# Performance work log

Measured on AMD Instinct MI355X. Metric: run time of the kernel, lower is better.

Reference implementation:

```python
import jax, jax.numpy as jnp
import numpy as np

GRID = 256
N_PER_ORG = 1536
N = 3 * N_PER_ORG
D = 256
H = 512
RADIUS = 5.0
FI_THRESHOLD = 0.5


def setup_inputs() -> dict:
    key = jax.random.key(0)
    ks = jax.random.split(key, 12)
    states = jax.random.normal(ks[0], (N, D), jnp.float32) * 0.1
    energies = jax.random.uniform(ks[1], (N,), jnp.float32, 0.2, 0.8)
    # radial resource distribution as in _init_resources
    c = GRID // 2
    yy, xx = jnp.meshgrid(jnp.arange(GRID, dtype=jnp.float32), jnp.arange(GRID, dtype=jnp.float32), indexing='ij')
    dist = jnp.sqrt((xx - c) ** 2 + (yy - c) ** 2)
    max_dist = jnp.sqrt(2.0) * GRID / 2
    resource_grid = jnp.maximum(0.0, 1.0 - dist / max_dist)
    sD, sH = 1.0 / np.sqrt(D), 1.0 / np.sqrt(H)
    W_out = jax.random.normal(ks[2], (3, D, H), jnp.float32) * sD
    W_in = jax.random.normal(ks[3], (3, D, H), jnp.float32) * sD
    W1 = jax.random.normal(ks[4], (3, D, H), jnp.float32) * sD
    W2 = jax.random.normal(ks[5], (3, H, D), jnp.float32) * sH
    b_out = jnp.zeros((3, H), jnp.float32)
    b_in = jnp.zeros((3, H), jnp.float32)
    b1 = jnp.zeros((3, H), jnp.float32)
    b2 = jnp.zeros((3, D), jnp.float32)
    roles = jax.random.randint(ks[6], (N,), 0, 3, jnp.int32)
    org_ids = jnp.repeat(jnp.arange(3, dtype=jnp.int32), N_PER_ORG)
    positions = jax.random.randint(ks[7], (N, 2), 0, GRID, jnp.int32)
    return {"states": states, "energies": energies, "resource_grid": resource_grid,
            "W_out": W_out, "b_out": b_out, "W_in": W_in, "b_in": b_in,
            "W1": W1, "b1": b1, "W2": W2, "b2": b2,
            "roles": roles, "org_ids": org_ids, "positions": positions}


def reference(states, energies, resource_grid, W_out, b_out, W_in, b_in, W1, b1, W2, b2, roles, org_ids, positions):
    n = states.shape[0]
    idx = jnp.arange(n)
    pos = positions.astype(jnp.float32)
    # neighbor mask: dist <= RADIUS, excluding self  [N,N]
    d2 = jnp.sum((pos[:, None, :] - pos[None, :, :]) ** 2, axis=-1)
    nb = (d2 <= RADIUS * RADIUS) & (~jnp.eye(n, dtype=bool))
    same_org = nb & (org_ids[:, None] == org_ids[None, :])
    other_org = nb & (org_ids[:, None] != org_ids[None, :])
    role0 = roles == 0
    role1 = roles == 1
    same_mass = jnp.sum(same_org & role0[None, :], axis=-1).astype(jnp.float32)
    same_fi = jnp.sum(same_org & role1[None, :], axis=-1).astype(jnp.float32)
    enemy_fi = jnp.sum(other_org & role1[None, :], axis=-1).astype(jnp.float32)
    # bidirectional influence (per-organism behavior nets)
    A = jnp.tanh(jnp.einsum('nd,kdh->knh', states, W_out) + b_out[:, None, :])  # [3,N,H]
    B = jnp.tanh(jnp.einsum('nd,kdh->knh', states, W_in) + b_in[:, None, :])
    scores = jnp.einsum('knh,kmh->knm', A, B) / np.sqrt(H)  # [3,N,N]
    sel_out = scores[org_ids, idx]                      # out_ij = score_{org_i}[i,j]
    sel_in = scores.transpose(0, 2, 1)[org_ids, idx]    # in_ij  = score_{org_i}[j,i]
    cnt = jnp.sum(same_org, axis=-1).astype(jnp.float32)
    denom = jnp.maximum(cnt, 1.0)
    out_mean = jnp.sum(sel_out * same_org, axis=-1) / denom
    in_mean = jnp.sum(sel_in * same_org, axis=-1) / denom
    has_nb = cnt > 0
    net_influence = jnp.where(has_nb, out_mean - in_mean, 0.0)
    # self similarity MLP, per-organism
    H1 = jnp.tanh(jnp.einsum('nd,kdh->knh', states, W1) + b1[:, None, :])
    SP = jnp.einsum('knh,khd->knd', H1, W2) + b2[:, None, :]
    sp = SP[org_ids, idx]  # [N,D]
    new_states = jnp.where(has_nb[:, None], states + 0.1 * sp, states)
    # energy update
    res = resource_grid[positions[:, 1], positions[:, 0]]
    e_fi = energies + 0.03 * same_mass + 0.02 * res - 0.04 * enemy_fi - 0.01
    e_mass = energies * 0.98 + 0.02 * (same_fi > 0).astype(jnp.float32) + 0.01 * res - 0.02 * enemy_fi
    new_energy = jnp.clip(jnp.where(role1, e_fi, e_mass), 0.0, 1.0)
    # role transitions (deterministic part of step())
    can_fi = (new_energy > FI_THRESHOLD) & (same_mass >= 2) & (same_fi == 0) & (enemy_fi == 0)
    r0_new = jnp.where(can_fi, 1, 0)
    loses = (same_mass < 1) | (new_energy < 0.15) | (enemy_fi > same_fi + 1)
    r1_new = jnp.where(loses, 0, 1)
    new_role_idx = jnp.where(role0, r0_new, jnp.where(role1, r1_new, roles))
    new_roles = jax.nn.one_hot(new_role_idx, 3, dtype=jnp.float32)
    return jnp.concatenate([new_states, net_influence[:, None], new_energy[:, None], new_roles], axis=-1)
```

## Files before the change

### kernel.cpp

```cpp
#include <hip/hip_runtime.h>

#define M_AG   4608
#define NPO    1536
#define D_DIM  256
#define H_DIM  512
#define NBIG   1536
#define GRID_SZ 256
#define NB_CAP 48

typedef __attribute__((ext_vector_type(8))) short short8;
typedef __attribute__((ext_vector_type(4))) float f32x4;
typedef unsigned short ushort_t;
typedef unsigned long long u64;

struct Args {
  const float *S, *W_out, *W_in, *W1, *W2, *b_out, *b_in, *b1, *b2;
  const float *energies, *resource_grid;
  const int *roles, *positions;
  ushort_t *Sc, *Wc, *W2c, *Abf, *Bbf, *Hc;
  int4 *stats;
  int *nbl;
  float *out;
};

__device__ __forceinline__ ushort_t f2bf(float f) {
  unsigned int u = __builtin_bit_cast(unsigned int, f);
  unsigned int r = (u + 0x7FFFu + ((u >> 16) & 1u)) >> 16;
  return (ushort_t)r;
}
__device__ __forceinline__ float bf2f(ushort_t u) {
  return __builtin_bit_cast(float, (unsigned int)u << 16);
}
__device__ __forceinline__ float tanh_fast(float x) {
  float e = __builtin_amdgcn_exp2f(x * 2.8853900817779268f);
  return 1.f - 2.f * __builtin_amdgcn_rcpf(e + 1.f);
}
__device__ __forceinline__ void gl_lds16(const ushort_t* g, ushort_t* l) {
  __builtin_amdgcn_global_load_lds(
      (const __attribute__((address_space(1))) unsigned int*)g,
      (__attribute__((address_space(3))) unsigned int*)l, 16, 0, 0);
}
#define VM0_BAR() do { asm volatile("s_waitcnt vmcnt(0)" ::: "memory"); \
                       __builtin_amdgcn_s_barrier(); } while (0)

__device__ __forceinline__ void pack_task(const Args& A, int task) {
  const int t = threadIdx.x;
  if (task < 576) {
    int idx = task * 256 + t;
    int kc = idx / M_AG, m = idx - kc * M_AG;
    const float* p = A.S + (size_t)m * D_DIM + kc * 8;
    ushort_t* d = A.Sc + (size_t)idx * 8;
#pragma unroll
    for (int j = 0; j < 8; ++j) d[j] = f2bf(p[j]);
  } else if (task < 1152) {
    int idx = (task - 576) * 256 + t;
    int org = idx / (32 * NBIG);
    int rem = idx - org * (32 * NBIG);
    int kc = rem / NBIG, n = rem - kc * NBIG;
    int which = n >> 9, nl = n & 511;
    const float* Wsel = (which == 0 ? A.W_out : which == 1 ? A.W_in : A.W1);
    const float* p = Wsel + (size_t)org * (D_DIM * H_DIM) + (size_t)kc * 8 * H_DIM + nl;
    ushort_t* d = A.Wc + (size_t)idx * 8;
#pragma unroll
    for (int j = 0; j < 8; ++j) d[j] = f2bf(p[(size_t)j * H_DIM]);
  } else {
    int idx = (task - 1152) * 256 + t;
    int org = idx / (64 * D_DIM);
    int rem = idx - org * (64 * D_DIM);
    int kc = rem >> 8, n = rem & 255;
    const float* p = A.W2 + (size_t)org * (H_DIM * D_DIM) + (size_t)kc * 8 * D_DIM + n;
    ushort_t* d = A.W2c + (size_t)idx * 8;
#pragma unroll
    for (int j = 0; j < 8; ++j) d[j] = f2bf(p[(size_t)j * D_DIM]);
  }
}

__device__ __forceinline__ void scan_task(const Args& A, int stask, char* smem) {
  const int t = threadIdx.x;
  int* pk = (int*)smem;
  u64* r0m = (u64*)(smem + 18432);
  u64* r1m = r0m + 72;
  for (int j = t; j < M_AG; j += 256) {
    int2 p2 = ((const int2*)A.positions)[j];
    pk[j] = p2.x | (p2.y << 8) | (A.roles[j] << 16);
  }
  __syncthreads();
  const int w = t >> 6, l = t & 63;
  for (int g = w; g < 72; g += 4) {
    int rj = pk[g * 64 + l] >> 16;
    u64 m0 = __ballot(rj == 0);
    u64 m1 = __ballot(rj == 1);
    if (l == 0) { r0m[g] = m0; r1m[g] = m1; }
  }
  __syncthreads();
  const int base_i = stask * 8;
#pragma unroll
  for (int rep = 0; rep < 2; ++rep) {
    const int i = base_i + rep * 4 + w;
    const int pi = pk[i];
    const int xi = pi & 255, yi = (pi >> 8) & 255;
    const int org = (i >= NPO) + (i >= 2 * NPO);
    const int olo = org * NPO, ohi = olo + NPO;
    int nbn = 0, mass = 0, fi = 0, enemy = 0;
    for (int bs = olo; bs < ohi; bs += 64) {
      int j = bs + l;
      int pj = pk[j];
      int dx = (pj & 255) - xi, dy = ((pj >> 8) & 255) - yi;
      bool in_r = (dx * dx + dy * dy <= 25) && (j != i);
      u64 ms = __ballot(in_r);
      if (ms) {
        int g = bs >> 6;
        mass += __popcll(ms & r0m[g]);
        fi   += __popcll(ms & r1m[g]);
        if (in_r) {
          int slot = nbn + __popcll(ms & ((1ull << l) - 1ull));
          if (slot < NB_CAP) A.nbl[i * NB_CAP + slot] = j;
        }
        nbn += __popcll(ms);
      }
    }
#pragma unroll
    for (int half = 0; half < 2; ++half) {
      const int lo = half ? ohi : 0;
      const int hi = half ? M_AG : olo;
      for (int bs = lo; bs < hi; bs += 64) {
        int pj = pk[bs + l];
        int dx = (pj & 255) - xi, dy = ((pj >> 8) & 255) - yi;
        u64 ms = __ballot(dx * dx + dy * dy <= 25);
        enemy += __popcll(ms & r1m[bs >> 6]);
      }
    }
    if (l == 0) A.stats[i] = make_int4(nbn, mass, fi, enemy);
  }
}

__device__ __forceinline__ void gemm_tile(const Args& A, int tix, char* smem) {
  ushort_t* As = (ushort_t*)smem;
  ushort_t* Bs = (ushort_t*)(smem + 16384);
  const int t = threadIdx.x;
  const int w = t >> 6, l = t & 63;
  const int wm = w >> 1, wn = w & 1;
  const int lr = l & 15, lg = l >> 4;
  const int bx = tix % 24, by = tix / 24;
  const int n0 = bx * 64, m0 = by * 64;
  const int org = m0 / NPO;
  const int which = n0 >> 9, nlb = n0 & 511;
  const int g0 = t >> 6, r0 = t & 63, g1 = 4 + g0;
  const size_t wbase = (size_t)org * 32;

  f32x4 acc[2][2] = {};

  auto STAGE = [&](int s, int p) {
    const int kg = s * 8;
    ushort_t* Ad = As + p * 4096;
    ushort_t* Bd = Bs + p * 4096;
    gl_lds16(A.Sc + ((size_t)(kg + g0) * M_AG + m0 + r0) * 8, Ad + (size_t)t * 8);
    gl_lds16(A.Sc + ((size_t)(kg + g1) * M_AG + m0 + r0) * 8, Ad + (size_t)(t + 256) * 8);
    gl_lds16(A.Wc + ((wbase + kg + g0) * NBIG + n0 + r0) * 8, Bd + (size_t)t * 8);
    gl_lds16(A.Wc + ((wbase + kg + g1) * NBIG + n0 + r0) * 8, Bd + (size_t)(t + 256) * 8);
  };

  STAGE(0, 0);
  VM0_BAR();
  for (int s = 0; s < 4; ++s) {
    const int p = s & 1;
    if (s < 3) STAGE(s + 1, p ^ 1);
    const short8* Ap = (const short8*)(As + p * 4096);
    const short8* Bp = (const short8*)(Bs + p * 4096);
    short8 af[2][2], bf_[2][2];
#pragma unroll
    for (int k2 = 0; k2 < 2; ++k2) {
#pragma unroll
      for (int mi = 0; mi < 2; ++mi)
        af[mi][k2] = Ap[(k2 * 4 + lg) * 64 + wm * 32 + mi * 16 + lr];
#pragma unroll
      for (int ni = 0; ni < 2; ++ni)
        bf_[ni][k2] = Bp[(k2 * 4 + lg) * 64 + wn * 32 + ni * 16 + lr];
    }
#pragma unroll
    for (int mi = 0; mi < 2; ++mi)
#pragma unroll
      for (int ni = 0; ni < 2; ++ni)
#pragma unroll
        for (int k2 = 0; k2 < 2; ++k2)
          acc[mi][ni] = __builtin_amdgcn_mfma_f32_16x16x32_bf16(
              af[mi][k2], bf_[ni][k2], acc[mi][ni], 0, 0, 0);
    VM0_BAR();
  }

  const float* bias = (which == 0 ? A.b_out : which == 1 ? A.b_in : A.b1) + (size_t)org * H_DIM;
  ushort_t* dst = (which == 0) ? A.Abf : A.Bbf;
#pragma unroll
  for (int ni = 0; ni < 2; ++ni) {
    const int nl = nlb + wn * 32 + ni * 16 + lr;
    const float bb = bias[nl];
#pragma unroll
    for (int mi = 0; mi < 2; ++mi)
#pragma unroll
      for (int r = 0; r < 4; ++r) {
        const int row = m0 + wm * 32 + mi * 16 + lg * 4 + r;
        ushort_t hv = f2bf(tanh_fast(acc[mi][ni][r] + bb));
        if (which < 2) dst[(size_t)row * H_DIM + nl] = hv;
        else           A.Hc[((size_t)(nl >> 3) * M_AG + row) * 8 + (nl & 7)] = hv;
      }
  }
}

__device__ __forceinline__ void sp_tile(const Args& A, int s_ix, char* smem) {
  ushort_t* As = (ushort_t*)smem;
  ushort_t* Bs = (ushort_t*)(smem + 16384);
  const int t = threadIdx.x;
  const int w = t >> 6, l = t & 63;
  const int wm = w >> 1, wn = w & 1;
  const int lr = l & 15, lg = l >> 4;
  const int bx = s_ix & 3, by = s_ix >> 2;
  const int n0 = bx * 64, m0 = by * 64;
  const int org = m0 / NPO;
  const int g0 = t >> 6, r0 = t & 63, g1 = 4 + g0;
  const size_t w2base = (size_t)org * 64;

  f32x4 acc[2][2] = {};

  auto STAGE = [&](int s, int p) {
    const int kg = s * 8;
    ushort_t* Ad = As + p * 4096;
    ushort_t* Bd = Bs + p * 4096;
    gl_lds16(A.Hc + ((size_t)(kg + g0) * M_AG + m0 + r0) * 8, Ad + (size_t)t * 8);
    gl_lds16(A.Hc + ((size_t)(kg + g1) * M_AG + m0 + r0) * 8, Ad + (size_t)(t + 256) * 8);
    gl_lds16(A.W2c + ((w2base + kg + g0) * D_DIM + n0 + r0) * 8, Bd + (size_t)t * 8);
    gl_lds16(A.W2c + ((w2base + kg + g1) * D_DIM + n0 + r0) * 8, Bd + (size_t)(t + 256) * 8);
  };

  STAGE(0, 0);
  VM0_BAR();
  for (int s = 0; s < 8; ++s) {
    const int p = s & 1;
    if (s < 7) STAGE(s + 1, p ^ 1);
    const short8* Ap = (const short8*)(As + p * 4096);
    const short8* Bp = (const short8*)(Bs + p * 4096);
    short8 af[2][2], bf_[2][2];
#pragma unroll
    for (int k2 = 0; k2 < 2; ++k2) {
#pragma unroll
      for (int mi = 0; mi < 2; ++mi)
        af[mi][k2] = Ap[(k2 * 4 + lg) * 64 + wm * 32 + mi * 16 + lr];
#pragma unroll
      for (int ni = 0; ni < 2; ++ni)
        bf_[ni][k2] = Bp[(k2 * 4 + lg) * 64 + wn * 32 + ni * 16 + lr];
    }
#pragma unroll
    for (int mi = 0; mi < 2; ++mi)
#pragma unroll
      for (int ni = 0; ni < 2; ++ni)
#pragma unroll
        for (int k2 = 0; k2 < 2; ++k2)
          acc[mi][ni] = __builtin_amdgcn_mfma_f32_16x16x32_bf16(
              af[mi][k2], bf_[ni][k2], acc[mi][ni], 0, 0, 0);
    VM0_BAR();
  }
#pragma unroll
  for (int mi = 0; mi < 2; ++mi)
#pragma unroll
    for (int r = 0; r < 4; ++r) {
      const int row = m0 + wm * 32 + mi * 16 + lg * 4 + r;
      const bool has = A.stats[row].x > 0;
#pragma unroll
      for (int ni = 0; ni < 2; ++ni) {
        const int col = n0 + wn * 32 + ni * 16 + lr;
        const float sv = A.S[(size_t)row * D_DIM + col];
        A.out[(size_t)row * 261 + col] =
            has ? sv + 0.1f * (acc[mi][ni][r] + A.b2[org * D_DIM + col]) : sv;
      }
    }
}

__device__ __forceinline__ void finish4(const Args& A, int ftask) {
  const int t = threadIdx.x;
  const int w = t >> 6, l = t & 63;
  const int i = ftask * 4 + w;
  const int4 stv = A.stats[i];
  const int cnt = stv.x, mass = stv.y, fi = stv.z, enemy = stv.w;
  float po = 0.f, pin = 0.f;
  if (cnt > 0) {
    short8 av = *(const short8*)(A.Abf + (size_t)i * H_DIM + l * 8);
    short8 bv = *(const short8*)(A.Bbf + (size_t)i * H_DIM + l * 8);
    const int nn = cnt < NB_CAP ? cnt : NB_CAP;
    for (int s = 0; s < nn; ++s) {
      const int j = A.nbl[i * NB_CAP + s];
      short8 bj = *(const short8*)(A.Bbf + (size_t)j * H_DIM + l * 8);
      short8 aj = *(const short8*)(A.Abf + (size_t)j * H_DIM + l * 8);
#pragma unroll
      for (int k2 = 0; k2 < 8; ++k2) {
        po  += bf2f((ushort_t)av[k2]) * bf2f((ushort_t)bj[k2]);
        pin += bf2f((ushort_t)bv[k2]) * bf2f((ushort_t)aj[k2]);
      }
    }
#pragma unroll
    for (int m2 = 1; m2 < 64; m2 <<= 1) {
      po  += __shfl_xor(po,  m2, 64);
      pin += __shfl_xor(pin, m2, 64);
    }
  }
  if (l == 0) {
    const float denom = fmaxf((float)cnt, 1.0f);
    const float invs = 0.044194173824159216f;
    const float ni_v = (cnt > 0) ? (po - pin) * invs / denom : 0.f;
    const int2 p2 = ((const int2*)A.positions)[i];
    const float res = A.resource_grid[p2.y * GRID_SZ + p2.x];
    const float e = A.energies[i];
    const int r = A.roles[i];
    float e_fi   = e + 0.03f * (float)mass + 0.02f * res - 0.04f * (float)enemy - 0.01f;
    float e_mass = e * 0.98f + 0.02f * ((fi > 0) ? 1.f : 0.f) + 0.01f * res - 0.02f * (float)enemy;
    float ne = (r == 1) ? e_fi : e_mass;
    ne = fminf(fmaxf(ne, 0.f), 1.f);
    const bool can_fi = (ne > 0.5f) && (mass >= 2) && (fi == 0) && (enemy == 0);
    const bool loses = (mass < 1) || (ne < 0.15f) || (enemy > fi + 1);
    const int nr = (r == 0) ? (can_fi ? 1 : 0) : ((r == 1) ? (loses ? 0 : 1) : r);
    float* orow = A.out + (size_t)i * 261;
    orow[256] = ni_v;
    orow[257] = ne;
    orow[258] = (nr == 0) ? 1.f : 0.f;
    orow[259] = (nr == 1) ? 1.f : 0.f;
    orow[260] = (nr == 2) ? 1.f : 0.f;
  }
}

__global__ __launch_bounds__(256) void k_p1(Args A) {
  pack_task(A, blockIdx.x);
}
__global__ __launch_bounds__(256) void k_p2(Args A) {
  __shared__ __align__(16) char smem[32768];
  if (blockIdx.x < 1728) gemm_tile(A, blockIdx.x, smem);
  else                   scan_task(A, blockIdx.x - 1728, smem);
}
__global__ __launch_bounds__(256) void k_p3(Args A) {
  __shared__ __align__(16) char smem[32768];
  if (blockIdx.x < 288) sp_tile(A, blockIdx.x, smem);
  else                  finish4(A, blockIdx.x - 288);
}

extern "C" void kernel_launch(void* const* d_in, const int* in_sizes, int n_in,
                              void* d_out, int out_size, void* d_ws, size_t ws_size,
                              hipStream_t stream) {
  char* ws = (char*)d_ws;
  Args a;
  a.S             = (const float*)d_in[0];
  a.energies      = (const float*)d_in[1];
  a.resource_grid = (const float*)d_in[2];
  a.W_out         = (const float*)d_in[3];
  a.b_out         = (const float*)d_in[4];
  a.W_in          = (const float*)d_in[5];
  a.b_in          = (const float*)d_in[6];
  a.W1            = (const float*)d_in[7];
  a.b1            = (const float*)d_in[8];
  a.W2            = (const float*)d_in[9];
  a.b2            = (const float*)d_in[10];
  a.roles         = (const int*)d_in[11];
  a.positions     = (const int*)d_in[13];
  a.Sc    = (ushort_t*)(ws);
  a.Wc    = (ushort_t*)(ws +  2359296);
  a.W2c   = (ushort_t*)(ws +  4718592);
  a.Hc    = (ushort_t*)(ws +  5505024);
  a.Abf   = (ushort_t*)(ws + 10223616);
  a.Bbf   = (ushort_t*)(ws + 14942208);
  a.stats = (int4*)    (ws + 19660800);
  a.nbl   = (int*)     (ws + 19734528);
  a.out   = (float*)d_out;

  k_p1<<<1344, 256, 0, stream>>>(a);
  k_p2<<<2304, 256, 0, stream>>>(a);
  k_p3<<<1440, 256, 0, stream>>>(a);
}
```

Baseline: 53.06 us.

## Fuse per-row self-similarity MLP with H1 in LDS and regroup kernels

Replaces the separate W1 GEMM tiles and the SP GEMM with one row-block MLP task. Each block computes tanh(S·W1) in chunks, stages H1 in LDS and immediately multiplies by W2, so the H1 workspace round trip through global memory disappears. The neighbour scan moves into the prep kernel alongside packing, and finalize gets its own kernel. The trade-off is that only 144 fused blocks run, and they read weights straight from global without LDS double buffering, which could leave a long tail.

```diff
diff --git a/kernel.cpp b/kernel.cpp
--- a/kernel.cpp
+++ b/kernel.cpp
@@ -17,7 +17,7 @@
   const float *S, *W_out, *W_in, *W1, *W2, *b_out, *b_in, *b1, *b2;
   const float *energies, *resource_grid;
   const int *roles, *positions;
-  ushort_t *Sc, *Wc, *W2c, *Abf, *Bbf, *Hc;
+  ushort_t *Sc, *Wc, *W2c, *Abf, *Bbf;
   int4 *stats;
   int *nbl;
   float *out;
@@ -141,7 +141,7 @@
   const int w = t >> 6, l = t & 63;
   const int wm = w >> 1, wn = w & 1;
   const int lr = l & 15, lg = l >> 4;
-  const int bx = tix % 24, by = tix / 24;
+  const int bx = tix & 15, by = tix >> 4;
   const int n0 = bx * 64, m0 = by * 64;
   const int org = m0 / NPO;
   const int which = n0 >> 9, nlb = n0 & 511;
@@ -188,7 +188,7 @@
     VM0_BAR();
   }
 
-  const float* bias = (which == 0 ? A.b_out : which == 1 ? A.b_in : A.b1) + (size_t)org * H_DIM;
+  const float* bias = (which == 0 ? A.b_out : A.b_in) + (size_t)org * H_DIM;
   ushort_t* dst = (which == 0) ? A.Abf : A.Bbf;
 #pragma unroll
   for (int ni = 0; ni < 2; ++ni) {
@@ -199,77 +199,115 @@
 #pragma unroll
       for (int r = 0; r < 4; ++r) {
         const int row = m0 + wm * 32 + mi * 16 + lg * 4 + r;
-        ushort_t hv = f2bf(tanh_fast(acc[mi][ni][r] + bb));
-        if (which < 2) dst[(size_t)row * H_DIM + nl] = hv;
-        else           A.Hc[((size_t)(nl >> 3) * M_AG + row) * 8 + (nl & 7)] = hv;
-      }
-  }
-}
-
-__device__ __forceinline__ void sp_tile(const Args& A, int s_ix, char* smem) {
-  ushort_t* As = (ushort_t*)smem;
-  ushort_t* Bs = (ushort_t*)(smem + 16384);
+        dst[(size_t)row * H_DIM + nl] = f2bf(tanh_fast(acc[mi][ni][r] + bb));
+      }
+  }
+}
+
+__device__ __forceinline__ void row_mlp(const Args& A, int blk, char* smem) {
+  ushort_t* Sres = (ushort_t*)smem;
+  ushort_t* H1c  = (ushort_t*)(smem + 16384);
   const int t = threadIdx.x;
   const int w = t >> 6, l = t & 63;
-  const int wm = w >> 1, wn = w & 1;
   const int lr = l & 15, lg = l >> 4;
-  const int bx = s_ix & 3, by = s_ix >> 2;
-  const int n0 = bx * 64, m0 = by * 64;
+  const int wn = w;
+  const int m0 = blk * 32;
   const int org = m0 / NPO;
-  const int g0 = t >> 6, r0 = t & 63, g1 = 4 + g0;
-  const size_t w2base = (size_t)org * 64;
-
-  f32x4 acc[2][2] = {};
-
-  auto STAGE = [&](int s, int p) {
-    const int kg = s * 8;
-    ushort_t* Ad = As + p * 4096;
-    ushort_t* Bd = Bs + p * 4096;
-    gl_lds16(A.Hc + ((size_t)(kg + g0) * M_AG + m0 + r0) * 8, Ad + (size_t)t * 8);
-    gl_lds16(A.Hc + ((size_t)(kg + g1) * M_AG + m0 + r0) * 8, Ad + (size_t)(t + 256) * 8);
-    gl_lds16(A.W2c + ((w2base + kg + g0) * D_DIM + n0 + r0) * 8, Bd + (size_t)t * 8);
-    gl_lds16(A.W2c + ((w2base + kg + g1) * D_DIM + n0 + r0) * 8, Bd + (size_t)(t + 256) * 8);
-  };
-
-  STAGE(0, 0);
+
+#pragma unroll
+  for (int j = 0; j < 4; ++j) {
+    int c = j * 256 + t;
+    int kg = c >> 5, row = c & 31;
+    gl_lds16(A.Sc + ((size_t)kg * M_AG + m0 + row) * 8, Sres + (size_t)c * 8);
+  }
   VM0_BAR();
-  for (int s = 0; s < 8; ++s) {
-    const int p = s & 1;
-    if (s < 7) STAGE(s + 1, p ^ 1);
-    const short8* Ap = (const short8*)(As + p * 4096);
-    const short8* Bp = (const short8*)(Bs + p * 4096);
-    short8 af[2][2], bf_[2][2];
-#pragma unroll
-    for (int k2 = 0; k2 < 2; ++k2) {
+
+  f32x4 sp[2][4] = {};
+  const short8* Sp = (const short8*)Sres;
+  const short8* Hp = (const short8*)H1c;
+
+#pragma unroll
+  for (int c = 0; c < 4; ++c) {
+    const int cbase = c * 128;
+    f32x4 a1[2][2] = {};
+#pragma unroll
+    for (int s = 0; s < 4; ++s) {
+      short8 bq[2][2];
+#pragma unroll
+      for (int ni = 0; ni < 2; ++ni)
+#pragma unroll
+        for (int k2 = 0; k2 < 2; ++k2)
+          bq[ni][k2] = *(const short8*)(A.Wc +
+              ((size_t)(org * 32 + s * 8 + k2 * 4 + lg) * NBIG +
+               1024 + cbase + wn * 32 + ni * 16 + lr) * 8);
+      short8 af[2][2];
 #pragma unroll
       for (int mi = 0; mi < 2; ++mi)
-        af[mi][k2] = Ap[(k2 * 4 + lg) * 64 + wm * 32 + mi * 16 + lr];
-#pragma unroll
-      for (int ni = 0; ni < 2; ++ni)
-        bf_[ni][k2] = Bp[(k2 * 4 + lg) * 64 + wn * 32 + ni * 16 + lr];
-    }
+#pragma unroll
+        for (int k2 = 0; k2 < 2; ++k2)
+          af[mi][k2] = Sp[(s * 8 + k2 * 4 + lg) * 32 + mi * 16 + lr];
+#pragma unroll
+      for (int mi = 0; mi < 2; ++mi)
+#pragma unroll
+        for (int ni = 0; ni < 2; ++ni)
+#pragma unroll
+          for (int k2 = 0; k2 < 2; ++k2)
+            a1[mi][ni] = __builtin_amdgcn_mfma_f32_16x16x32_bf16(
+                af[mi][k2], bq[ni][k2], a1[mi][ni], 0, 0, 0);
+    }
+    __syncthreads();
 #pragma unroll
     for (int mi = 0; mi < 2; ++mi)
 #pragma unroll
-      for (int ni = 0; ni < 2; ++ni)
+      for (int ni = 0; ni < 2; ++ni) {
+        const int col = wn * 32 + ni * 16 + lr;
+        const float bb = A.b1[org * H_DIM + cbase + col];
+#pragma unroll
+        for (int r = 0; r < 4; ++r) {
+          const int row = mi * 16 + lg * 4 + r;
+          H1c[((size_t)(col >> 3) * 32 + row) * 8 + (col & 7)] =
+              f2bf(tanh_fast(a1[mi][ni][r] + bb));
+        }
+      }
+    __syncthreads();
+#pragma unroll
+    for (int s2 = 0; s2 < 2; ++s2) {
+      short8 bq[4][2];
+#pragma unroll
+      for (int ni = 0; ni < 4; ++ni)
 #pragma unroll
         for (int k2 = 0; k2 < 2; ++k2)
-          acc[mi][ni] = __builtin_amdgcn_mfma_f32_16x16x32_bf16(
-              af[mi][k2], bf_[ni][k2], acc[mi][ni], 0, 0, 0);
-    VM0_BAR();
+          bq[ni][k2] = *(const short8*)(A.W2c +
+              ((size_t)(org * 64 + c * 16 + s2 * 8 + k2 * 4 + lg) * D_DIM +
+               wn * 64 + ni * 16 + lr) * 8);
+      short8 af[2][2];
+#pragma unroll
+      for (int mi = 0; mi < 2; ++mi)
+#pragma unroll
+        for (int k2 = 0; k2 < 2; ++k2)
+          af[mi][k2] = Hp[(s2 * 8 + k2 * 4 + lg) * 32 + mi * 16 + lr];
+#pragma unroll
+      for (int mi = 0; mi < 2; ++mi)
+#pragma unroll
+        for (int ni = 0; ni < 4; ++ni)
+#pragma unroll
+          for (int k2 = 0; k2 < 2; ++k2)
+            sp[mi][ni] = __builtin_amdgcn_mfma_f32_16x16x32_bf16(
+                af[mi][k2], bq[ni][k2], sp[mi][ni], 0, 0, 0);
+    }
   }
 #pragma unroll
   for (int mi = 0; mi < 2; ++mi)
 #pragma unroll
     for (int r = 0; r < 4; ++r) {
-      const int row = m0 + wm * 32 + mi * 16 + lg * 4 + r;
+      const int row = m0 + mi * 16 + lg * 4 + r;
       const bool has = A.stats[row].x > 0;
 #pragma unroll
-      for (int ni = 0; ni < 2; ++ni) {
-        const int col = n0 + wn * 32 + ni * 16 + lr;
+      for (int ni = 0; ni < 4; ++ni) {
+        const int col = wn * 64 + ni * 16 + lr;
         const float sv = A.S[(size_t)row * D_DIM + col];
         A.out[(size_t)row * 261 + col] =
-            has ? sv + 0.1f * (acc[mi][ni][r] + A.b2[org * D_DIM + col]) : sv;
+            has ? sv + 0.1f * (sp[mi][ni][r] + A.b2[org * D_DIM + col]) : sv;
       }
     }
 }
@@ -325,18 +363,18 @@
   }
 }
 
-__global__ __launch_bounds__(256) void k_p1(Args A) {
-  pack_task(A, blockIdx.x);
-}
-__global__ __launch_bounds__(256) void k_p2(Args A) {
+__global__ __launch_bounds__(256) void k_prep(Args A) {
+  __shared__ __align__(16) char smem[19584];
+  if (blockIdx.x < 1344) pack_task(A, blockIdx.x);
+  else                   scan_task(A, blockIdx.x - 1344, smem);
+}
+__global__ __launch_bounds__(256) void k_main(Args A) {
   __shared__ __align__(16) char smem[32768];
-  if (blockIdx.x < 1728) gemm_tile(A, blockIdx.x, smem);
-  else                   scan_task(A, blockIdx.x - 1728, smem);
-}
-__global__ __launch_bounds__(256) void k_p3(Args A) {
-  __shared__ __align__(16) char smem[32768];
-  if (blockIdx.x < 288) sp_tile(A, blockIdx.x, smem);
-  else                  finish4(A, blockIdx.x - 288);
+  if (blockIdx.x < 144) row_mlp(A, blockIdx.x, smem);
+  else                  gemm_tile(A, blockIdx.x - 144, smem);
+}
+__global__ __launch_bounds__(256) void k_fin(Args A) {
+  finish4(A, blockIdx.x);
 }
 
 extern "C" void kernel_launch(void* const* d_in, const int* in_sizes, int n_in,
@@ -360,14 +398,13 @@
   a.Sc    = (ushort_t*)(ws);
   a.Wc    = (ushort_t*)(ws +  2359296);
   a.W2c   = (ushort_t*)(ws +  4718592);
-  a.Hc    = (ushort_t*)(ws +  5505024);
-  a.Abf   = (ushort_t*)(ws + 10223616);
-  a.Bbf   = (ushort_t*)(ws + 14942208);
-  a.stats = (int4*)    (ws + 19660800);
-  a.nbl   = (int*)     (ws + 19734528);
+  a.Abf   = (ushort_t*)(ws +  5505024);
+  a.Bbf   = (ushort_t*)(ws + 10223616);
+  a.stats = (int4*)    (ws + 14942208);
+  a.nbl   = (int*)     (ws + 15015936);
   a.out   = (float*)d_out;
 
-  k_p1<<<1344, 256, 0, stream>>>(a);
-  k_p2<<<2304, 256, 0, stream>>>(a);
-  k_p3<<<1440, 256, 0, stream>>>(a);
-}
+  k_prep<<<1920, 256, 0, stream>>>(a);
+  k_main<<<1296, 256, 0, stream>>>(a);
+  k_fin <<<1152, 256, 0, stream>>>(a);
+}
```

Result: slower. 59.93 us (+12.9%).
